# Kernel tuning notes

Measured on AMD Instinct MI355X. Metric: run time of the kernel, lower is better.

Reference implementation:

```python
import jax, jax.numpy as jnp
import numpy as np

HEADS = 12
EMBED = 768
HEAD_DIM = EMBED // HEADS


def setup_inputs() -> dict:
    key = jax.random.key(0)
    kx, kw, kb = jax.random.split(key, 3)
    x = jax.random.normal(kx, (8, 1024, EMBED), dtype=jnp.float32)
    # nn.Linear(embed, 3*embed): weight (3E, E), bias (3E,)
    W_qkv = jax.random.normal(kw, (3 * EMBED, EMBED), dtype=jnp.float32) * (1.0 / np.sqrt(EMBED))
    b_qkv = jax.random.normal(kb, (3 * EMBED,), dtype=jnp.float32) * 0.01
    return {"x": x, "W_qkv": W_qkv, "b_qkv": b_qkv}


def reference(x, W_qkv, b_qkv):
    b, n, e = x.shape
    qkv = x @ W_qkv.T + b_qkv                       # (b, n, 3E)
    qkv = qkv.reshape(b, n, HEADS, 3 * HEAD_DIM)    # (b, n, h, 3d)
    q, k, v = jnp.split(qkv, 3, axis=-1)            # each (b, n, h, d)
    scores = jnp.einsum('bihd,bjhd->bijh', q, k) / np.sqrt(HEAD_DIM)
    attn = jax.nn.softmax(scores, axis=-2)          # softmax over keys j (dim=-2)
    out = jnp.einsum('bijh,bjhd->bihd', attn, v)
    return out.reshape(b, n, e)
```

## Files before the change

### kernel.cpp

```cpp
#include <hip/hip_runtime.h>
#include <hip/hip_bf16.h>
#include <cstdint>

#define BATCH 8
#define SEQ   1024
#define EMB   768
#define HEADS 12
#define HDIM  64
#define C3    2304
#define MROWS (BATCH*SEQ)

typedef __attribute__((ext_vector_type(8))) short bf16x8;
typedef __attribute__((ext_vector_type(4))) short bf16x4;
typedef __attribute__((ext_vector_type(4))) float f32x4;

static __device__ inline short f2bf(float f) {
    union { float f; uint32_t u; } v; v.f = f;
    uint32_t u = v.u + 0x7fff + ((v.u >> 16) & 1);
    return (short)(u >> 16);
}

static __device__ inline void gload_lds16(const short* g, short* l) {
    __builtin_amdgcn_global_load_lds(
        (const __attribute__((address_space(1))) void*)g,
        (__attribute__((address_space(3))) void*)l, 16, 0, 0);
}

__global__ __launch_bounds__(256) void f32_to_bf16(const float* __restrict__ in,
                                                   short* __restrict__ out, int n8) {
    int i = blockIdx.x * 256 + threadIdx.x;
    if (i >= n8) return;
    float4 v0 = ((const float4*)in)[i * 2];
    float4 v1 = ((const float4*)in)[i * 2 + 1];
    bf16x8 o = { f2bf(v0.x), f2bf(v0.y), f2bf(v0.z), f2bf(v0.w),
                 f2bf(v1.x), f2bf(v1.y), f2bf(v1.z), f2bf(v1.w) };
    ((bf16x8*)out)[i] = o;
}

__global__ __launch_bounds__(256) void qkv_gemm_mfma(const short* __restrict__ xb,
                                                     const short* __restrict__ Wb,
                                                     const float* __restrict__ bias,
                                                     short* __restrict__ qkvb) {
    __shared__ short As[128 * 32];
    __shared__ short Bs[128 * 32];

    const int bx = blockIdx.x;
    const int by = blockIdx.y;
    const int t = threadIdx.x;
    const int w = t >> 6;
    const int lane = t & 63;
    const int c = lane & 15, q = lane >> 4;
    const int m0 = by * 128, n0 = bx * 128;
    const int wm = (w & 1) * 64, wn = (w >> 1) * 64;

    const int srow = lane >> 2;
    const int scol = (lane & 3) * 8;
    const short* ga0 = xb + (size_t)(m0 + w * 16 + srow) * EMB + scol;
    const short* ga1 = xb + (size_t)(m0 + 64 + w * 16 + srow) * EMB + scol;
    const short* gb0 = Wb + (size_t)(n0 + w * 16 + srow) * EMB + scol;
    const short* gb1 = Wb + (size_t)(n0 + 64 + w * 16 + srow) * EMB + scol;
    short* la0 = &As[(w * 16) * 32];
    short* la1 = &As[(64 + w * 16) * 32];
    short* lb0 = &Bs[(w * 16) * 32];
    short* lb1 = &Bs[(64 + w * 16) * 32];

    f32x4 acc[4][4] = {};

    for (int k0 = 0; k0 < EMB; k0 += 32) {
        __syncthreads();
        gload_lds16(ga0 + k0, la0);
        gload_lds16(ga1 + k0, la1);
        gload_lds16(gb0 + k0, lb0);
        gload_lds16(gb1 + k0, lb1);
        __syncthreads();

        bf16x8 a[4], b[4];
        #pragma unroll
        for (int mt = 0; mt < 4; ++mt)
            a[mt] = *(bf16x8*)&As[(wm + mt * 16 + c) * 32 + q * 8];
        #pragma unroll
        for (int nt = 0; nt < 4; ++nt)
            b[nt] = *(bf16x8*)&Bs[(wn + nt * 16 + c) * 32 + q * 8];
        #pragma unroll
        for (int mt = 0; mt < 4; ++mt)
            #pragma unroll
            for (int nt = 0; nt < 4; ++nt)
                acc[mt][nt] = __builtin_amdgcn_mfma_f32_16x16x32_bf16(
                    a[mt], b[nt], acc[mt][nt], 0, 0, 0);
    }

    float bsv[4], scl[4];
    #pragma unroll
    for (int nt = 0; nt < 4; ++nt) {
        int n = n0 + wn + nt * 16 + c;
        bsv[nt] = bias[n];
        scl[nt] = ((n % 192) < 64) ? 0.125f : 1.0f;
    }
    #pragma unroll
    for (int mt = 0; mt < 4; ++mt)
        #pragma unroll
        for (int nt = 0; nt < 4; ++nt)
            #pragma unroll
            for (int r = 0; r < 4; ++r) {
                int m = m0 + wm + mt * 16 + q * 4 + r;
                int n = n0 + wn + nt * 16 + c;
                float v = (acc[mt][nt][r] + bsv[nt]) * scl[nt];
                qkvb[(size_t)m * C3 + n] = f2bf(v);
            }
}

__global__ __launch_bounds__(256) void v_transpose(const short* __restrict__ qkvb,
                                                   short* __restrict__ vt) {
    __shared__ int Lt[64][65];

    const int bh = blockIdx.x;
    const int jt = blockIdx.y;
    const int b = bh / HEADS, h = bh % HEADS;
    const int t = threadIdx.x;
    const int j0 = jt * 64;
    const size_t base = (size_t)b * SEQ * C3 + (size_t)h * 192 + 128;

    #pragma unroll
    for (int p = 0; p < 2; ++p) {
        int idx = p * 256 + t;
        int j = idx >> 3, d0 = (idx & 7) * 8;
        bf16x8 v = *(const bf16x8*)(qkvb + base + (size_t)(j0 + j) * C3 + d0);
        #pragma unroll
        for (int u = 0; u < 8; ++u)
            Lt[d0 + u][j] = (int)(unsigned short)v[u];
    }
    __syncthreads();
    #pragma unroll
    for (int p = 0; p < 2; ++p) {
        int idx = p * 256 + t;
        int d = idx >> 3, c8 = (idx & 7) * 8;
        bf16x8 o;
        #pragma unroll
        for (int u = 0; u < 8; ++u)
            o[u] = (short)Lt[d][c8 + u];
        *(bf16x8*)(vt + ((size_t)bh * 64 + d) * SEQ + j0 + c8) = o;
    }
}

#define LDP 72

__global__ __launch_bounds__(256, 4) void attn_mfma(const short* __restrict__ qkvb,
                                                    const short* __restrict__ vt,
                                                    float* __restrict__ out) {
    __shared__ short Ks[64][LDP];
    __shared__ short Vt[64][LDP];
    __shared__ short Ps[64][LDP];

    const int bx   = blockIdx.x;
    const int qt   = bx & 15;
    const int h    = (bx >> 4) % HEADS;
    const int b    = bx / (16 * HEADS);
    const int t    = threadIdx.x;
    const int w    = t >> 6;
    const int lane = t & 63;
    const int c    = lane & 15;
    const int q    = lane >> 4;
    const int i0   = qt * 64;

    const size_t base = (size_t)b * SEQ * C3 + (size_t)h * 192;
    const short* vtb = vt + (size_t)(b * HEADS + h) * 64 * SEQ;

    #pragma unroll
    for (int p = 0; p < 2; ++p) {
        int idx = p * 256 + t;
        int i = idx >> 3, d0 = (idx & 7) << 3;
        *(bf16x8*)&Ps[i][d0] =
            *(const bf16x8*)(qkvb + base + (size_t)(i0 + i) * C3 + d0);
    }
    __syncthreads();
    const bf16x8 aq0 = *(bf16x8*)&Ps[w * 16 + c][q * 8];
    const bf16x8 aq1 = *(bf16x8*)&Ps[w * 16 + c][32 + q * 8];

    f32x4 o[4] = {{0.f,0.f,0.f,0.f},{0.f,0.f,0.f,0.f},
                  {0.f,0.f,0.f,0.f},{0.f,0.f,0.f,0.f}};
    float l_acc = 0.f;

    for (int kt = 0; kt < 16; ++kt) {
        const int j0 = kt * 64;
        __syncthreads();
        #pragma unroll
        for (int p = 0; p < 2; ++p) {
            int idx = p * 256 + t;
            int j = idx >> 3, d0 = (idx & 7) << 3;
            *(bf16x8*)&Ks[j][d0] =
                *(const bf16x8*)(qkvb + base + 64 + (size_t)(j0 + j) * C3 + d0);
        }
        #pragma unroll
        for (int p = 0; p < 2; ++p) {
            int idx = p * 256 + t;
            int d = idx >> 3, j8 = (idx & 7) << 3;
            *(bf16x8*)&Vt[d][j8] =
                *(const bf16x8*)(vtb + (size_t)d * SEQ + j0 + j8);
        }
        __syncthreads();

        f32x4 s[4];
        #pragma unroll
        for (int mt = 0; mt < 4; ++mt) {
            bf16x8 a0 = *(bf16x8*)&Ks[mt * 16 + c][q * 8];
            bf16x8 a1 = *(bf16x8*)&Ks[mt * 16 + c][32 + q * 8];
            f32x4 acc = {0.f, 0.f, 0.f, 0.f};
            acc = __builtin_amdgcn_mfma_f32_16x16x32_bf16(a0, aq0, acc, 0, 0, 0);
            acc = __builtin_amdgcn_mfma_f32_16x16x32_bf16(a1, aq1, acc, 0, 0, 0);
            s[mt] = acc;
        }

        #pragma unroll
        for (int mt = 0; mt < 4; ++mt) {
            float p0 = __expf(s[mt][0]);
            float p1 = __expf(s[mt][1]);
            float p2 = __expf(s[mt][2]);
            float p3 = __expf(s[mt][3]);
            l_acc += (p0 + p1) + (p2 + p3);
            bf16x4 pw = { f2bf(p0), f2bf(p1), f2bf(p2), f2bf(p3) };
            *(bf16x4*)&Ps[w * 16 + c][mt * 16 + 4 * q] = pw;
        }

        bf16x8 ap0 = *(bf16x8*)&Ps[w * 16 + c][q * 8];
        bf16x8 ap1 = *(bf16x8*)&Ps[w * 16 + c][32 + q * 8];
        #pragma unroll
        for (int dt = 0; dt < 4; ++dt) {
            bf16x8 b0 = *(bf16x8*)&Vt[dt * 16 + c][q * 8];
            bf16x8 b1 = *(bf16x8*)&Vt[dt * 16 + c][32 + q * 8];
            o[dt] = __builtin_amdgcn_mfma_f32_16x16x32_bf16(ap0, b0, o[dt], 0, 0, 0);
            o[dt] = __builtin_amdgcn_mfma_f32_16x16x32_bf16(ap1, b1, o[dt], 0, 0, 0);
        }
    }

    l_acc += __shfl_xor(l_acc, 16, 64);
    l_acc += __shfl_xor(l_acc, 32, 64);
    float linv[4];
    #pragma unroll
    for (int r = 0; r < 4; ++r)
        linv[r] = 1.0f / __shfl(l_acc, 4 * q + r, 64);

    #pragma unroll
    for (int dt = 0; dt < 4; ++dt)
        #pragma unroll
        for (int r = 0; r < 4; ++r) {
            int i = w * 16 + q * 4 + r;
            out[((size_t)b * SEQ + i0 + i) * EMB + h * HDIM + dt * 16 + c]
                = o[dt][r] * linv[r];
        }
}

extern "C" void kernel_launch(void* const* d_in, const int* in_sizes, int n_in,
                              void* d_out, int out_size, void* d_ws, size_t ws_size,
                              hipStream_t stream) {
    const float* x    = (const float*)d_in[0];
    const float* W    = (const float*)d_in[1];
    const float* bias = (const float*)d_in[2];
    float* out = (float*)d_out;

    short* xb   = (short*)d_ws;
    short* Wb   = xb + (size_t)MROWS * EMB;
    short* qkvb = Wb + (size_t)C3 * EMB;
    short* vt   = qkvb + (size_t)MROWS * C3;

    f32_to_bf16<<<(MROWS * EMB / 8 + 255) / 256, 256, 0, stream>>>(x, xb, MROWS * EMB / 8);
    f32_to_bf16<<<(C3 * EMB / 8 + 255) / 256, 256, 0, stream>>>(W, Wb, C3 * EMB / 8);

    dim3 g1(C3 / 128, MROWS / 128);
    qkv_gemm_mfma<<<g1, 256, 0, stream>>>(xb, Wb, bias, qkvb);

    dim3 g2(BATCH * HEADS, SEQ / 64);
    v_transpose<<<g2, 256, 0, stream>>>(qkvb, vt);

    attn_mfma<<<BATCH * HEADS * (SEQ / 64), 256, 0, stream>>>(qkvb, vt, out);
}
```

Measured before the change: 182.3 us.

## Double-buffer QKV GEMM LDS tiles and switch to 32x32x16 MFMA with padded layout

The QKV projection GEMM now double-buffers its LDS tiles, so the global-to-LDS loads for the next k-step are issued while the current step computes, and one of the two barriers per iteration is removed. It switches from 16x16x32 to 32x32x16 bf16 MFMA with 2x2 tiles per wave. LDS chunks are padded (stride 528 shorts) to reduce bank conflicts. The epilogue is remapped to the 32x32 accumulator layout. LDS use doubles, which may reduce occupancy.

New measurement: 183.8 us. Within noise of the previous version (+0.8%).

```diff
diff --git a/kernel.cpp b/kernel.cpp
--- a/kernel.cpp
+++ b/kernel.cpp
@@ -10,9 +10,10 @@
 #define C3    2304
 #define MROWS (BATCH*SEQ)
 
-typedef __attribute__((ext_vector_type(8))) short bf16x8;
-typedef __attribute__((ext_vector_type(4))) short bf16x4;
-typedef __attribute__((ext_vector_type(4))) float f32x4;
+typedef __attribute__((ext_vector_type(8)))  short bf16x8;
+typedef __attribute__((ext_vector_type(4)))  short bf16x4;
+typedef __attribute__((ext_vector_type(4)))  float f32x4;
+typedef __attribute__((ext_vector_type(16))) float f32x16;
 
 static __device__ inline short f2bf(float f) {
     union { float f; uint32_t u; } v; v.f = f;
@@ -37,19 +38,20 @@
     ((bf16x8*)out)[i] = o;
 }
 
+#define CHK 528
+
 __global__ __launch_bounds__(256) void qkv_gemm_mfma(const short* __restrict__ xb,
                                                      const short* __restrict__ Wb,
                                                      const float* __restrict__ bias,
                                                      short* __restrict__ qkvb) {
-    __shared__ short As[128 * 32];
-    __shared__ short Bs[128 * 32];
+    __shared__ short As[2][8 * CHK];
+    __shared__ short Bs[2][8 * CHK];
 
     const int bx = blockIdx.x;
     const int by = blockIdx.y;
     const int t = threadIdx.x;
     const int w = t >> 6;
     const int lane = t & 63;
-    const int c = lane & 15, q = lane >> 4;
     const int m0 = by * 128, n0 = bx * 128;
     const int wm = (w & 1) * 64, wn = (w >> 1) * 64;
 
@@ -59,54 +61,78 @@
     const short* ga1 = xb + (size_t)(m0 + 64 + w * 16 + srow) * EMB + scol;
     const short* gb0 = Wb + (size_t)(n0 + w * 16 + srow) * EMB + scol;
     const short* gb1 = Wb + (size_t)(n0 + 64 + w * 16 + srow) * EMB + scol;
-    short* la0 = &As[(w * 16) * 32];
-    short* la1 = &As[(64 + w * 16) * 32];
-    short* lb0 = &Bs[(w * 16) * 32];
-    short* lb1 = &Bs[(64 + w * 16) * 32];
-
-    f32x4 acc[4][4] = {};
-
-    for (int k0 = 0; k0 < EMB; k0 += 32) {
+
+    const int l5  = lane >> 5;
+    const int r31 = lane & 31;
+    const int rlo = lane & 15;
+    const int rhi = (lane >> 4) & 1;
+    int aoff[2], boff[2];
+    #pragma unroll
+    for (int mt = 0; mt < 2; ++mt)
+        aoff[mt] = ((wm >> 4) + 2 * mt + rhi) * CHK + rlo * 32 + l5 * 8;
+    #pragma unroll
+    for (int nt = 0; nt < 2; ++nt)
+        boff[nt] = ((wn >> 4) + 2 * nt + rhi) * CHK + rlo * 32 + l5 * 8;
+
+    f32x16 acc[2][2] = {};
+
+    gload_lds16(ga0, &As[0][w * CHK]);
+    gload_lds16(ga1, &As[0][(4 + w) * CHK]);
+    gload_lds16(gb0, &Bs[0][w * CHK]);
+    gload_lds16(gb1, &Bs[0][(4 + w) * CHK]);
+    __syncthreads();
+
+    for (int kt = 0; kt < 24; ++kt) {
+        const int cur = kt & 1, nxt = cur ^ 1;
+        if (kt < 23) {
+            const int ko = (kt + 1) * 32;
+            gload_lds16(ga0 + ko, &As[nxt][w * CHK]);
+            gload_lds16(ga1 + ko, &As[nxt][(4 + w) * CHK]);
+            gload_lds16(gb0 + ko, &Bs[nxt][w * CHK]);
+            gload_lds16(gb1 + ko, &Bs[nxt][(4 + w) * CHK]);
+        }
+        bf16x8 a[2][2], b[2][2];
+        #pragma unroll
+        for (int mt = 0; mt < 2; ++mt)
+            #pragma unroll
+            for (int s = 0; s < 2; ++s)
+                a[mt][s] = *(bf16x8*)&As[cur][aoff[mt] + s * 16];
+        #pragma unroll
+        for (int nt = 0; nt < 2; ++nt)
+            #pragma unroll
+            for (int s = 0; s < 2; ++s)
+                b[nt][s] = *(bf16x8*)&Bs[cur][boff[nt] + s * 16];
+        #pragma unroll
+        for (int mt = 0; mt < 2; ++mt)
+            #pragma unroll
+            for (int nt = 0; nt < 2; ++nt)
+                #pragma unroll
+                for (int s = 0; s < 2; ++s)
+                    acc[mt][nt] = __builtin_amdgcn_mfma_f32_32x32x16_bf16(
+                        a[mt][s], b[nt][s], acc[mt][nt], 0, 0, 0);
         __syncthreads();
-        gload_lds16(ga0 + k0, la0);
-        gload_lds16(ga1 + k0, la1);
-        gload_lds16(gb0 + k0, lb0);
-        gload_lds16(gb1 + k0, lb1);
-        __syncthreads();
-
-        bf16x8 a[4], b[4];
-        #pragma unroll
-        for (int mt = 0; mt < 4; ++mt)
-            a[mt] = *(bf16x8*)&As[(wm + mt * 16 + c) * 32 + q * 8];
-        #pragma unroll
-        for (int nt = 0; nt < 4; ++nt)
-            b[nt] = *(bf16x8*)&Bs[(wn + nt * 16 + c) * 32 + q * 8];
-        #pragma unroll
-        for (int mt = 0; mt < 4; ++mt)
-            #pragma unroll
-            for (int nt = 0; nt < 4; ++nt)
-                acc[mt][nt] = __builtin_amdgcn_mfma_f32_16x16x32_bf16(
-                    a[mt], b[nt], acc[mt][nt], 0, 0, 0);
-    }
-
-    float bsv[4], scl[4];
-    #pragma unroll
-    for (int nt = 0; nt < 4; ++nt) {
-        int n = n0 + wn + nt * 16 + c;
+    }
+
+    float bsv[2], scl[2];
+    #pragma unroll
+    for (int nt = 0; nt < 2; ++nt) {
+        int n = n0 + wn + nt * 32 + r31;
         bsv[nt] = bias[n];
         scl[nt] = ((n % 192) < 64) ? 0.125f : 1.0f;
     }
     #pragma unroll
-    for (int mt = 0; mt < 4; ++mt)
-        #pragma unroll
-        for (int nt = 0; nt < 4; ++nt)
+    for (int mt = 0; mt < 2; ++mt)
+        #pragma unroll
+        for (int nt = 0; nt < 2; ++nt) {
+            int n = n0 + wn + nt * 32 + r31;
             #pragma unroll
-            for (int r = 0; r < 4; ++r) {
-                int m = m0 + wm + mt * 16 + q * 4 + r;
-                int n = n0 + wn + nt * 16 + c;
-                float v = (acc[mt][nt][r] + bsv[nt]) * scl[nt];
+            for (int reg = 0; reg < 16; ++reg) {
+                int row = (reg & 3) + 8 * (reg >> 2) + 4 * l5;
+                int m = m0 + wm + mt * 32 + row;
+                float v = (acc[mt][nt][reg] + bsv[nt]) * scl[nt];
                 qkvb[(size_t)m * C3 + n] = f2bf(v);
             }
+        }
 }
 
 __global__ __launch_bounds__(256) void v_transpose(const short* __restrict__ qkvb,
```
